# Performance work log

Hardware: AMD Instinct MI355X
Metric: run time of the kernel (lower is better)

Reference implementation:

```python
import jax, jax.numpy as jnp
import numpy as np

B, S, HID, H = 1, 4096, 1024, 16
D = HID // H  # 64
SCALE = D ** -0.5
NEG = -1e30


def setup_inputs() -> dict:
    key = jax.random.key(0)
    ks = jax.random.split(key, 8)
    hidden_states = jax.random.normal(ks[0], (B, S, HID), dtype=jnp.float32)
    attention_mask = jax.random.randint(ks[1], (B, S), 0, 2, dtype=jnp.int32)
    # Linear weights stored as [in, out] so y = x @ W + b
    init = lambda k, shape: jax.random.normal(k, shape, dtype=jnp.float32) * (HID ** -0.5)
    return {
        "hidden_states": hidden_states,
        "attention_mask": attention_mask,
        "Wq": init(ks[2], (HID, HID)), "bq": jnp.zeros((HID,), jnp.float32),
        "Wk": init(ks[3], (HID, HID)), "bk": jnp.zeros((HID,), jnp.float32),
        "Wv": init(ks[4], (HID, HID)), "bv": jnp.zeros((HID,), jnp.float32),
    }


def reference(hidden_states, attention_mask, Wq, bq, Wk, bk, Wv, bv):
    x = hidden_states
    q = (x @ Wq + bq).reshape(B, S, H, D)
    k = (x @ Wk + bk).reshape(B, S, H, D)
    v = (x @ Wv + bv).reshape(B, S, H, D)
    mask = attention_mask.astype(bool)  # [B, S] over keys
    # scores: [B, H, Sq, Sk]
    scores = jnp.einsum("bqhd,bkhd->bhqk", q, k) * SCALE
    scores = jnp.where(mask[:, None, None, :], scores, NEG)
    attn = jax.nn.softmax(scores, axis=-1)
    ctx = jnp.einsum("bhqk,bkhd->bqhd", attn, v).reshape(B, S, HID)
    return (ctx,)
```

## Files before the change

### kernel.cpp

```cpp
#include <hip/hip_runtime.h>
#include <stdint.h>

#define S_    4096
#define HID_  1024
#define H_    16
#define N3    3072
#define NT    64
#define SCALE_f 0.125f
#define NEG_f  (-1e30f)
#define SCL2  (0.125f * 1.44269504089f)

typedef __attribute__((ext_vector_type(4))) float f32x4;
typedef __attribute__((ext_vector_type(8))) short bf16x8;
typedef __attribute__((ext_vector_type(4))) short bf16x4;

#define MFMA16(a,b,c) __builtin_amdgcn_mfma_f32_16x16x32_bf16((a),(b),(c),0,0,0)
#define GLDS16(g,l) __builtin_amdgcn_global_load_lds( \
    (__attribute__((address_space(1))) void*)(g), \
    (__attribute__((address_space(3))) void*)(l), 16, 0, 0)

__device__ __forceinline__ f32x4 MFMA16K16(bf16x4 a, bf16x4 b, f32x4 c){
#if __has_builtin(__builtin_amdgcn_mfma_f32_16x16x16bf16_1k)
  return __builtin_amdgcn_mfma_f32_16x16x16bf16_1k(a, b, c, 0, 0, 0);
#else
  asm volatile("v_mfma_f32_16x16x16_bf16 %0, %1, %2, %0" : "+v"(c) : "v"(a), "v"(b));
  return c;
#endif
}

__device__ __forceinline__ unsigned short f2b(float f){
  union { float f; uint32_t u; } a; a.f = f;
  uint32_t u = a.u;
  return (unsigned short)((u + 0x7fffu + ((u >> 16) & 1u)) >> 16);
}

__global__ __launch_bounds__(256) void cvt_x_kern(const float* __restrict__ x,
                                                  unsigned short* __restrict__ xb){
  int i = (blockIdx.x * 256 + threadIdx.x) * 4;
  const float4 v = *(const float4*)(x + i);
  ushort4 o;
  o.x = f2b(v.x); o.y = f2b(v.y); o.z = f2b(v.z); o.w = f2b(v.w);
  *(ushort4*)(xb + i) = o;
}

__global__ __launch_bounds__(256) void cvt_w_t_kern(const float* __restrict__ W,
                                                    unsigned short* __restrict__ wt,
                                                    int nbase){
  __shared__ float tile[32][33];
  int k0 = blockIdx.x * 32, n0 = blockIdx.y * 32;
  int tx = threadIdx.x, ty = threadIdx.y;
  for (int i = 0; i < 32; i += 8)
    tile[ty + i][tx] = W[(k0 + ty + i) * HID_ + n0 + tx];
  __syncthreads();
  for (int i = 0; i < 32; i += 8)
    wt[(nbase + n0 + ty + i) * HID_ + k0 + tx] = f2b(tile[tx][ty + i]);
}

#define BM 128
#define BN 128
#define BK 32
__global__ __launch_bounds__(256) void gemm_qkv_kern(
    const unsigned short* __restrict__ xb,
    const unsigned short* __restrict__ wt,
    const float* __restrict__ bq, const float* __restrict__ bk,
    const float* __restrict__ bv,
    unsigned short* __restrict__ qkv)
{
  __shared__ unsigned short As[BM * BK];
  __shared__ unsigned short Bs[BN * BK];
  int tid = threadIdx.x;
  int lane = tid & 63, wid = tid >> 6;
  int g = lane >> 4, l16 = lane & 15;
  int m0 = blockIdx.x * BM, n0 = blockIdx.y * BN;
  int wm = (wid >> 1) * 64, wn = (wid & 1) * 64;

  f32x4 acc[4][4];
  f32x4 z = {0.f, 0.f, 0.f, 0.f};
  for (int mi = 0; mi < 4; mi++) for (int ni = 0; ni < 4; ni++) acc[mi][ni] = z;

  for (int kt = 0; kt < HID_; kt += BK) {
    __syncthreads();
    for (int i = 0; i < 2; i++) {
      int flat = tid * 8 + i * 2048;
      int m = flat >> 5, k = flat & 31;
      GLDS16(xb + (m0 + m) * HID_ + kt + k, As + flat);
    }
    for (int i = 0; i < 2; i++) {
      int flat = tid * 8 + i * 2048;
      int n = flat >> 5, k = flat & 31;
      GLDS16(wt + (n0 + n) * HID_ + kt + k, Bs + flat);
    }
    __syncthreads();
    bf16x8 a[4], b[4];
    for (int mi = 0; mi < 4; mi++)
      a[mi] = *(const bf16x8*)(As + (wm + mi * 16 + l16) * BK + g * 8);
    for (int ni = 0; ni < 4; ni++)
      b[ni] = *(const bf16x8*)(Bs + (wn + ni * 16 + l16) * BK + g * 8);
    for (int mi = 0; mi < 4; mi++)
      for (int ni = 0; ni < 4; ni++)
        acc[mi][ni] = MFMA16(a[mi], b[ni], acc[mi][ni]);
  }

  for (int mi = 0; mi < 4; mi++)
    for (int ni = 0; ni < 4; ni++) {
      int col = n0 + wn + ni * 16 + l16;
      float bias = (col < 1024) ? bq[col] : ((col < 2048) ? bk[col - 1024] : bv[col - 2048]);
      for (int r = 0; r < 4; r++) {
        int row = m0 + wm + mi * 16 + g * 4 + r;
        qkv[row * N3 + col] = f2b(acc[mi][ni][r] + bias);
      }
    }
}

__global__ __launch_bounds__(256) void vt_kern(const unsigned short* __restrict__ qkv,
                                               unsigned short* __restrict__ vt){
  __shared__ unsigned short tl[64][72];
  int h = blockIdx.y, k0 = blockIdx.x * 64, tid = threadIdx.x;
  int key = tid >> 2, dq = (tid & 3) * 16;
  const unsigned short* src = qkv + (size_t)(k0 + key) * N3 + 2048 + h * 64 + dq;
  *(bf16x8*)&tl[key][dq]     = *(const bf16x8*)src;
  *(bf16x8*)&tl[key][dq + 8] = *(const bf16x8*)(src + 8);
  __syncthreads();
  int d = tid >> 2, kq = (tid & 3) * 16;
  unsigned short* dst = vt + ((size_t)h * 64 + d) * S_ + k0 + kq;
  bf16x8 o0, o1;
  for (int j = 0; j < 8; j++) { o0[j] = tl[kq + j][d]; o1[j] = tl[kq + 8 + j][d]; }
  *(bf16x8*)dst = o0; *(bf16x8*)(dst + 8) = o1;
}

__global__ void maskbits_kern(const int* __restrict__ mask,
                              unsigned long long* __restrict__ mb){
  int t = threadIdx.x;
  unsigned long long wv = 0;
  for (int j = 0; j < 64; j++)
    wv |= (unsigned long long)(mask[t * 64 + j] != 0) << j;
  mb[t] = wv;
}

__global__ __launch_bounds__(256, 4) void attn_kern(
    const unsigned short* __restrict__ qkv,
    const unsigned short* __restrict__ vt,
    const unsigned long long* __restrict__ mb,
    float* __restrict__ out)
{
  __shared__ unsigned short Ks[2][64 * 64];
  __shared__ unsigned short Vs[2][64 * 64];
  __shared__ unsigned long long MaskL[NT];

  int tid = threadIdx.x, lane = tid & 63, w = tid >> 6;
  int g = lane >> 4, l16 = lane & 15;
  int bid = blockIdx.x;
  int swz = (bid & 7) * 128 + (bid >> 3);
  int h = swz >> 6, q0 = (swz & 63) * 64;

  const unsigned short* Q = qkv + h * 64;
  const unsigned short* K = qkv + 1024 + h * 64;
  const unsigned short* V = vt + (size_t)h * 64 * S_;

  if (tid < NT) MaskL[tid] = mb[tid];

  bf16x8 qf[2];
  for (int ks = 0; ks < 2; ks++)
    qf[ks] = *(const bf16x8*)(Q + (size_t)(q0 + w * 16 + l16) * N3 + ks * 32 + g * 8);

  f32x4 po[4];
  f32x4 z = {0.f, 0.f, 0.f, 0.f};
  for (int db = 0; db < 4; db++) po[db] = z;
  float m_l = -__builtin_inff(), l_l = 0.f;

  int swl = (l16 & 7) << 4;
  int rof[2];
  for (int ks = 0; ks < 2; ks++) rof[ks] = ((ks * 64 + g * 16) ^ swl) >> 1;
  int vof[4];
  for (int nb = 0; nb < 4; nb++) vof[nb] = ((nb * 32 + g * 8) ^ swl) >> 1;

  auto STAGE = [&](int b, int t) {
    int k0 = t * 64;
    for (int i = 0; i < 2; i++) {
      int F = tid * 16 + i * 4096;
      int row = F >> 7, inner = F & 127;
      int sin = (inner ^ ((row & 7) << 4)) >> 1;
      GLDS16(K + (size_t)(k0 + row) * N3 + sin, &Ks[b][F >> 1]);
      GLDS16(V + (size_t)row * S_ + k0 + sin,    &Vs[b][F >> 1]);
    }
  };

  STAGE(0, 0);
  asm volatile("s_waitcnt vmcnt(0) lgkmcnt(0)" ::: "memory");
  __builtin_amdgcn_s_barrier();

  int cur = 0;
  for (int t = 0; t < NT; t++) {
    if (t + 1 < NT) STAGE(cur ^ 1, t + 1);
    unsigned long long mw = MaskL[t];

    f32x4 sc[4];
    for (int nb = 0; nb < 4; nb++) sc[nb] = z;
    for (int nb = 0; nb < 4; nb++) {
      int rb = (nb * 16 + l16) * 64;
      for (int ks = 0; ks < 2; ks++) {
        bf16x8 kf = *(const bf16x8*)(&Ks[cur][rb + rof[ks]]);
        sc[nb] = MFMA16(kf, qf[ks], sc[nb]);
      }
    }

    float pl[4][4];
    for (int nb = 0; nb < 4; nb++) {
      unsigned mn = (unsigned)((mw >> (nb * 16 + g * 4)) & 0xFull);
      for (int r = 0; r < 4; r++)
        pl[nb][r] = ((mn >> r) & 1u) ? sc[nb][r] * SCL2 : NEG_f;
    }

    float pmax = pl[0][0];
    for (int nb = 0; nb < 4; nb++)
      for (int r = 0; r < 4; r++) pmax = fmaxf(pmax, pl[nb][r]);
    pmax = fmaxf(pmax, __shfl_xor(pmax, 16, 64));
    pmax = fmaxf(pmax, __shfl_xor(pmax, 32, 64));

    if (__ballot(pmax > m_l + 8.f)) {
      float mnew = fmaxf(m_l, pmax);
      float alpha = __builtin_amdgcn_exp2f(m_l - mnew);
      for (int db = 0; db < 4; db++) po[db] *= alpha;
      l_l *= alpha;
      m_l = mnew;
    }

    float rsum = 0.f;
    bf16x4 pb[4];
    for (int nb = 0; nb < 4; nb++)
      for (int r = 0; r < 4; r++) {
        float p = __builtin_amdgcn_exp2f(pl[nb][r] - m_l);
        rsum += p;
        pb[nb][r] = (short)f2b(p);
      }
    rsum += __shfl_xor(rsum, 16, 64);
    rsum += __shfl_xor(rsum, 32, 64);
    l_l += rsum;

    for (int db = 0; db < 4; db++) {
      int rb = (db * 16 + l16) * 64;
      for (int nb = 0; nb < 4; nb++) {
        bf16x4 va = *(const bf16x4*)(&Vs[cur][rb + vof[nb]]);
        po[db] = MFMA16K16(va, pb[nb], po[db]);
      }
    }

    asm volatile("s_waitcnt vmcnt(0) lgkmcnt(0)" ::: "memory");
    __builtin_amdgcn_s_barrier();
    cur ^= 1;
  }

  float inv = 1.0f / l_l;
  int q = q0 + w * 16 + l16;
  for (int db = 0; db < 4; db++) {
    f32x4 v = po[db] * inv;
    *(f32x4*)(out + (size_t)q * HID_ + h * 64 + db * 16 + g * 4) = v;
  }
}

extern "C" void kernel_launch(void* const* d_in, const int* in_sizes, int n_in,
                              void* d_out, int out_size, void* d_ws, size_t ws_size,
                              hipStream_t stream) {
  const float* x    = (const float*)d_in[0];
  const int*   mask = (const int*)d_in[1];
  const float* Wq   = (const float*)d_in[2];
  const float* bq   = (const float*)d_in[3];
  const float* Wk   = (const float*)d_in[4];
  const float* bk   = (const float*)d_in[5];
  const float* Wv   = (const float*)d_in[6];
  const float* bv   = (const float*)d_in[7];
  float* out = (float*)d_out;

  uint8_t* ws = (uint8_t*)d_ws;
  unsigned short* xb  = (unsigned short*)ws;
  unsigned short* wt  = (unsigned short*)(ws + (8u  << 20));
  unsigned short* qkv = (unsigned short*)(ws + (14u << 20));
  unsigned short* vt  = (unsigned short*)ws;
  unsigned long long* mb = (unsigned long long*)(ws + (8u << 20));

  cvt_x_kern<<<(S_ * HID_) / (256 * 4), 256, 0, stream>>>(x, xb);
  dim3 tg(HID_ / 32, HID_ / 32);
  cvt_w_t_kern<<<tg, dim3(32, 8), 0, stream>>>(Wq, wt, 0);
  cvt_w_t_kern<<<tg, dim3(32, 8), 0, stream>>>(Wk, wt, 1024);
  cvt_w_t_kern<<<tg, dim3(32, 8), 0, stream>>>(Wv, wt, 2048);
  gemm_qkv_kern<<<dim3(S_ / BM, N3 / BN), 256, 0, stream>>>(xb, wt, bq, bk, bv, qkv);
  vt_kern<<<dim3(S_ / 64, H_), 256, 0, stream>>>(qkv, vt);
  maskbits_kern<<<1, 64, 0, stream>>>(mask, mb);
  attn_kern<<<S_ / 64 * H_, 256, 0, stream>>>(qkv, vt, mb, out);
}
```

Before: 271.5 us.

## Move key masking into zeroed V rows and streamline the softmax inner loop

Masked keys are now handled by zeroing their V rows during the transpose kernel and by a 0/1 multiply on the row sum, so the per-element select to NEG is removed from the attention loop. The max is taken on raw scores with v_max3, the scale is folded into one FMA before exp2, and probabilities are packed with hardware bf16 pack conversion. This cuts VALU work in the softmax, but the running max now includes masked-key scores, which can change numerical range, and a raw-score rescale threshold is used instead.

```diff
diff --git a/kernel.cpp b/kernel.cpp
--- a/kernel.cpp
+++ b/kernel.cpp
@@ -9,6 +9,7 @@
 #define SCALE_f 0.125f
 #define NEG_f  (-1e30f)
 #define SCL2  (0.125f * 1.44269504089f)
+#define THRRAW 44.3614f
 
 typedef __attribute__((ext_vector_type(4))) float f32x4;
 typedef __attribute__((ext_vector_type(8))) short bf16x8;
@@ -26,6 +27,13 @@
   asm volatile("v_mfma_f32_16x16x16_bf16 %0, %1, %2, %0" : "+v"(c) : "v"(a), "v"(b));
   return c;
 #endif
+}
+
+__device__ __forceinline__ float max3f(float a, float b, float c){
+  float d; asm("v_max3_f32 %0, %1, %2, %3" : "=v"(d) : "v"(a), "v"(b), "v"(c)); return d;
+}
+__device__ __forceinline__ uint32_t cvtpk(float lo, float hi){
+  uint32_t r; asm("v_cvt_pk_bf16_f32 %0, %1, %2" : "=v"(r) : "v"(lo), "v"(hi)); return r;
 }
 
 __device__ __forceinline__ unsigned short f2b(float f){
@@ -113,13 +121,20 @@
 }
 
 __global__ __launch_bounds__(256) void vt_kern(const unsigned short* __restrict__ qkv,
+                                               const int* __restrict__ mask,
                                                unsigned short* __restrict__ vt){
   __shared__ unsigned short tl[64][72];
   int h = blockIdx.y, k0 = blockIdx.x * 64, tid = threadIdx.x;
   int key = tid >> 2, dq = (tid & 3) * 16;
   const unsigned short* src = qkv + (size_t)(k0 + key) * N3 + 2048 + h * 64 + dq;
-  *(bf16x8*)&tl[key][dq]     = *(const bf16x8*)src;
-  *(bf16x8*)&tl[key][dq + 8] = *(const bf16x8*)(src + 8);
+  bf16x8 v0 = *(const bf16x8*)src;
+  bf16x8 v1 = *(const bf16x8*)(src + 8);
+  if (mask[k0 + key] == 0) {
+    bf16x8 zz = {0,0,0,0,0,0,0,0};
+    v0 = zz; v1 = zz;
+  }
+  *(bf16x8*)&tl[key][dq]     = v0;
+  *(bf16x8*)&tl[key][dq + 8] = v1;
   __syncthreads();
   int d = tid >> 2, kq = (tid & 3) * 16;
   unsigned short* dst = vt + ((size_t)h * 64 + d) * S_ + k0 + kq;
@@ -193,6 +208,7 @@
   for (int t = 0; t < NT; t++) {
     if (t + 1 < NT) STAGE(cur ^ 1, t + 1);
     unsigned long long mw = MaskL[t];
+    uint32_t mlo = (uint32_t)mw, mhi = (uint32_t)(mw >> 32);
 
     f32x4 sc[4];
     for (int nb = 0; nb < 4; nb++) sc[nb] = z;
@@ -204,35 +220,42 @@
       }
     }
 
-    float pl[4][4];
-    for (int nb = 0; nb < 4; nb++) {
-      unsigned mn = (unsigned)((mw >> (nb * 16 + g * 4)) & 0xFull);
-      for (int r = 0; r < 4; r++)
-        pl[nb][r] = ((mn >> r) & 1u) ? sc[nb][r] * SCL2 : NEG_f;
-    }
-
-    float pmax = pl[0][0];
-    for (int nb = 0; nb < 4; nb++)
-      for (int r = 0; r < 4; r++) pmax = fmaxf(pmax, pl[nb][r]);
+    float m0 = max3f(sc[0][0], sc[0][1], sc[0][2]);
+    float m1 = max3f(sc[0][3], sc[1][0], sc[1][1]);
+    float m2 = max3f(sc[1][2], sc[1][3], sc[2][0]);
+    float m3 = max3f(sc[2][1], sc[2][2], sc[2][3]);
+    float m4 = max3f(sc[3][0], sc[3][1], sc[3][2]);
+    float m5 = max3f(m0, m1, sc[3][3]);
+    float m6 = max3f(m2, m3, m4);
+    float pmax = fmaxf(m5, m6);
     pmax = fmaxf(pmax, __shfl_xor(pmax, 16, 64));
     pmax = fmaxf(pmax, __shfl_xor(pmax, 32, 64));
 
-    if (__ballot(pmax > m_l + 8.f)) {
+    if (__ballot(pmax > m_l + THRRAW)) {
       float mnew = fmaxf(m_l, pmax);
-      float alpha = __builtin_amdgcn_exp2f(m_l - mnew);
+      float alpha = __builtin_amdgcn_exp2f((m_l - mnew) * SCL2);
       for (int db = 0; db < 4; db++) po[db] *= alpha;
       l_l *= alpha;
       m_l = mnew;
     }
+    float negmsc = m_l * (-SCL2);
 
     float rsum = 0.f;
     bf16x4 pb[4];
-    for (int nb = 0; nb < 4; nb++)
+    for (int nb = 0; nb < 4; nb++) {
+      uint32_t msrc = (nb < 2) ? mlo : mhi;
+      float pr[4];
       for (int r = 0; r < 4; r++) {
-        float p = __builtin_amdgcn_exp2f(pl[nb][r] - m_l);
-        rsum += p;
-        pb[nb][r] = (short)f2b(p);
+        float p = __builtin_amdgcn_exp2f(__builtin_fmaf(sc[nb][r], SCL2, negmsc));
+        float b = (float)((msrc >> ((nb & 1) * 16 + g * 4 + r)) & 1u);
+        rsum = __builtin_fmaf(p, b, rsum);
+        pr[r] = p;
       }
+      union { uint32_t w[2]; bf16x4 v; } pu;
+      pu.w[0] = cvtpk(pr[0], pr[1]);
+      pu.w[1] = cvtpk(pr[2], pr[3]);
+      pb[nb] = pu.v;
+    }
     rsum += __shfl_xor(rsum, 16, 64);
     rsum += __shfl_xor(rsum, 32, 64);
     l_l += rsum;
@@ -284,7 +307,7 @@
   cvt_w_t_kern<<<tg, dim3(32, 8), 0, stream>>>(Wk, wt, 1024);
   cvt_w_t_kern<<<tg, dim3(32, 8), 0, stream>>>(Wv, wt, 2048);
   gemm_qkv_kern<<<dim3(S_ / BM, N3 / BN), 256, 0, stream>>>(xb, wt, bq, bk, bv, qkv);
-  vt_kern<<<dim3(S_ / 64, H_), 256, 0, stream>>>(qkv, vt);
+  vt_kern<<<dim3(S_ / 64, H_), 256, 0, stream>>>(qkv, mask, vt);
   maskbits_kern<<<1, 64, 0, stream>>>(mask, mb);
   attn_kern<<<S_ / 64 * H_, 256, 0, stream>>>(qkv, vt, mb, out);
 }
```

Result: faster. 261.8 us (-3.6%).
